# Optimization experiments

Measured on AMD Instinct MI355X. Metric: run time of the kernel, lower is better.

Reference implementation:

```python
import jax, jax.numpy as jnp
import numpy as np

B, Q, K = 4, 256, 1024          # batch, query_len, key_len
DQ, DK, DV, H = 512, 512, 512, 256  # query/key/value dims, num_hiddens


def setup_inputs() -> dict:
    key = jax.random.key(0)
    ks = jax.random.split(key, 7)
    return {
        "queries": jax.random.normal(ks[0], (B, Q, DQ), jnp.float32),
        "keys": jax.random.normal(ks[1], (B, K, DK), jnp.float32),
        "values": jax.random.normal(ks[2], (B, K, DV), jnp.float32),
        "valid_lens": jax.random.randint(ks[3], (B,), 1, K + 1),
        "Wq": jax.random.normal(ks[4], (H, DQ), jnp.float32) / np.sqrt(DQ).astype(np.float32),
        "Wk": jax.random.normal(ks[5], (H, DK), jnp.float32) / np.sqrt(DK).astype(np.float32),
        "wv": jax.random.normal(ks[6], (H,), jnp.float32) / np.sqrt(H).astype(np.float32),
    }


def reference(queries, keys, values, valid_lens, Wq, Wk, wv):
    # Linear projections (bias=False), torch Linear weight layout (out, in)
    q = jnp.einsum("bqd,hd->bqh", queries, Wq)          # (B, Q, H)
    k = jnp.einsum("bkd,hd->bkh", keys, Wk)             # (B, K, H)
    # Broadcast add -> tanh -> scalar score per (q, k) pair
    feats = jnp.tanh(q[:, :, None, :] + k[:, None, :, :])  # (B, Q, K, H)
    scores = jnp.einsum("bqkh,h->bqk", feats, wv)           # (B, Q, K)
    # masked_softmax with 1D valid_lens: mask applies along key axis per batch
    kv_len = scores.shape[-1]
    mask = jnp.arange(kv_len)[None, None, :] < valid_lens[:, None, None]  # (B,1,K)
    scores = jnp.where(mask, scores, jnp.float32(-1e6))
    attn = jax.nn.softmax(scores, axis=-1)               # (B, Q, K)
    # dropout is identity in eval mode
    return jnp.einsum("bqk,bkv->bqv", attn, values)      # (B, Q, DV)
```

## Files before the change

kernel.cpp:

```cpp
#include <hip/hip_runtime.h>
#include <stdint.h>


#define NB 4
#define NQ 256
#define NK 1024
#define ND 512
#define NH 256
#define QROWS 4
#define PJR 16
#define PJH 64

#define C2L2E 2.8853900817779268f
#define L2E   1.4426950408889634f

typedef float v2f __attribute__((ext_vector_type(2)));

__device__ void ff_vldec(const int* p, int* v) {
  bool ok = true;
  for (int i = 0; i < 4; ++i) { int x = p[i]; if (x < 1 || x > NK) ok = false; }
  if (ok) { for (int i = 0; i < 4; ++i) v[i] = p[i]; return; }
  ok = true;
  for (int i = 0; i < 4; ++i) {
    if (p[2 * i + 1] != 0) ok = false;
    int x = p[2 * i]; if (x < 1 || x > NK) ok = false;
  }
  if (ok) { for (int i = 0; i < 4; ++i) v[i] = p[2 * i]; return; }
  ok = true;
  for (int i = 0; i < 4; ++i) {
    union { int i; float f; } u; u.i = p[i];
    if (!(u.f >= 1.0f && u.f <= 1024.0f && u.f == floorf(u.f))) ok = false;
  }
  if (ok) {
    for (int i = 0; i < 4; ++i) { union { int i; float f; } u; u.i = p[i]; v[i] = (int)u.f; }
    return;
  }
  ok = true;
  for (int i = 0; i < 4; ++i) {
    union { long long l; double d; } u;
    u.l = ((long long)p[2 * i + 1] << 32) | (unsigned int)p[2 * i];
    if (!(u.d >= 1.0 && u.d <= 1024.0 && u.d == floor(u.d))) ok = false;
  }
  if (ok) {
    for (int i = 0; i < 4; ++i) {
      union { long long l; double d; } u;
      u.l = ((long long)p[2 * i + 1] << 32) | (unsigned int)p[2 * i];
      v[i] = (int)u.d;
    }
    return;
  }
  const uint16_t* hh = (const uint16_t*)p;
  const short*    s  = (const short*)p;
  ok = true;
  for (int i = 0; i < 4; ++i) { int x = s[i]; if (x < 1 || x > NK) ok = false; }
  if (ok) { for (int i = 0; i < 4; ++i) v[i] = s[i]; return; }
  ok = true;
  for (int i = 0; i < 4; ++i) {
    union { uint16_t u; _Float16 h; } u; u.u = hh[i];
    float f = (float)u.h;
    if (!(f >= 1.0f && f <= 1024.0f && f == floorf(f))) ok = false;
  }
  if (ok) {
    for (int i = 0; i < 4; ++i) {
      union { uint16_t u; _Float16 h; } u; u.u = hh[i];
      v[i] = (int)(float)u.h;
    }
    return;
  }
  ok = true;
  for (int i = 0; i < 4; ++i) {
    union { uint32_t u; float f; } u; u.u = ((uint32_t)hh[i]) << 16;
    if (!(u.f >= 1.0f && u.f <= 1028.0f)) ok = false;
  }
  if (ok) {
    for (int i = 0; i < 4; ++i) {
      union { uint32_t u; float f; } u; u.u = ((uint32_t)hh[i]) << 16;
      int x = (int)(u.f + 0.5f); if (x > NK) x = NK; v[i] = x;
    }
    return;
  }
  for (int i = 0; i < 4; ++i) v[i] = NK;
}

__global__ __launch_bounds__(256) void ff_wt(
    const float* __restrict__ Wq, const float* __restrict__ Wk,
    float* __restrict__ WTq, float* __restrict__ WTk)
{
  const int idx = blockIdx.x * 256 + threadIdx.x;
  const int d4 = idx & 127, h = idx >> 7;
  const float* src = blockIdx.y ? Wk : Wq;
  float*       dst = blockIdx.y ? WTk : WTq;
  float4 w = *(const float4*)(src + (size_t)h * ND + d4 * 4);
  w.x *= C2L2E; w.y *= C2L2E; w.z *= C2L2E; w.w *= C2L2E;
  *(float4*)(dst + ((size_t)d4 * NH + h) * 4) = w;
}

__global__ __launch_bounds__(256) void ff_proj(
    const float* __restrict__ q_in, const float* __restrict__ k_in,
    const float* __restrict__ WTq, const float* __restrict__ WTk,
    float* __restrict__ qp, float* __restrict__ kp)
{
  __shared__ float xs[PJR * ND];
  const int t  = threadIdx.x;
  const int rg = blockIdx.x >> 2;
  const int h0 = (blockIdx.x & 3) * PJH;
  const int gr0 = rg * PJR;
  const bool isq = gr0 < NB * NQ;
  const float* xin = isq ? (q_in + (size_t)gr0 * ND)
                         : (k_in + (size_t)(gr0 - NB * NQ) * ND);
  const float4* wt4 = (const float4*)(isq ? WTq : WTk);

  #pragma unroll
  for (int i = 0; i < 8; ++i)
    ((float4*)xs)[t + 256 * i] = ((const float4*)xin)[t + 256 * i];
  __syncthreads();

  const int L  = t & 63;
  const int rw = t >> 6;
  float a0 = 0.f, a1 = 0.f, a2 = 0.f, a3 = 0.f;
  const float4* xr = (const float4*)xs + (size_t)(4 * rw) * 128;

  #pragma unroll 4
  for (int d4 = 0; d4 < ND / 4; ++d4) {
    float4 w  = wt4[(size_t)d4 * NH + h0 + L];
    float4 x0 = xr[d4];
    float4 x1 = xr[128 + d4];
    float4 x2 = xr[256 + d4];
    float4 x3 = xr[384 + d4];
    a0 += w.x*x0.x + w.y*x0.y + w.z*x0.z + w.w*x0.w;
    a1 += w.x*x1.x + w.y*x1.y + w.z*x1.z + w.w*x1.w;
    a2 += w.x*x2.x + w.y*x2.y + w.z*x2.z + w.w*x2.w;
    a3 += w.x*x3.x + w.y*x3.y + w.z*x3.z + w.w*x3.w;
  }
  a0 = __builtin_amdgcn_exp2f(a0);
  a1 = __builtin_amdgcn_exp2f(a1);
  a2 = __builtin_amdgcn_exp2f(a2);
  a3 = __builtin_amdgcn_exp2f(a3);

  if (isq) {
    const int h = h0 + L;
    float* o = qp + (size_t)(gr0 + 4 * rw) * NH + h;
    o[0] = a0; o[NH] = a1; o[2 * NH] = a2; o[3 * NH] = a3;
  } else {
    __syncthreads();
    float* trs = xs;
    *(float4*)&trs[L * 16 + 4 * rw] = make_float4(a0, a1, a2, a3);
    __syncthreads();
    const int kl = t & 15, jl = t >> 4;
    const int g0 = gr0 - NB * NQ;
    const int bb = g0 >> 10, kg0 = g0 & (NK - 1);
    const int j0 = (blockIdx.x & 3) * 16;
    float4 o4 = make_float4(trs[(4*jl+0)*16 + kl], trs[(4*jl+1)*16 + kl],
                            trs[(4*jl+2)*16 + kl], trs[(4*jl+3)*16 + kl]);
    ((float4*)kp)[((size_t)bb * 64 + j0 + jl) * 1024 + kg0 + kl] = o4;
  }
}

__global__ __launch_bounds__(1024) void ff_attn4(
    const float* __restrict__ qp, const float* __restrict__ kp,
    const float* __restrict__ vals, const int* __restrict__ vlraw,
    const float* __restrict__ wvp, float* __restrict__ pvpart,
    float* __restrict__ Sg)
{
  __shared__ float  qs[QROWS * NH];
  __shared__ float4 wspp[NH / 2];
  __shared__ float  stp[2 * 256 * 4];
  __shared__ float  psum[16];
  __shared__ float  part[2 * 4 * 512];

  const int t  = threadIdx.x;
  const int ck = blockIdx.x;
  const int q0 = blockIdx.y * QROWS;
  const int b  = blockIdx.z;

  {
    qs[t] = qp[((size_t)b * NQ + q0) * NH + t];
    if (t < NH / 2) {
      float w0 = wvp[2 * t], w1 = wvp[2 * t + 1];
      wspp[t] = make_float4(-2.0f * w0, -2.0f * w1, -2.0f * (w0 + w1), 0.0f);
    }
  }
  __syncthreads();

  int vls[4];
  ff_vldec(vlraw, vls);
  const int vl = vls[b];

  const int kk = t & 255, rh = (t >> 8) & 1, hs = t >> 9;
  v2f acc = {0.f, 0.f};
  {
    const float4* kvp = (const float4*)kp + ((size_t)b * 64) * 1024
                      + (ck * 256 + kk);
    const float* q0p = qs + (2 * rh) * NH;
    const float* q1p = qs + (2 * rh + 1) * NH;
    #pragma unroll 4
    for (int jj = 0; jj < 32; ++jj) {
      const int j = hs * 32 + jj;
      float4 K4 = kvp[(size_t)j << 10];
      float4 A0 = *(const float4*)(q0p + 4 * j);
      float4 A1 = *(const float4*)(q1p + 4 * j);
      float4 wa = wspp[2 * j];
      float4 wb = wspp[2 * j + 1];
      v2f one; one.x = 1.0f; one.y = 1.0f;
      {
        v2f a;  a.x  = A0.x * K4.x; a.y  = A1.x * K4.x;
        v2f b2; b2.x = A0.y * K4.y; b2.y = A1.y * K4.y;
        v2f D = (one + a) * (one + b2);
        v2f N;   N.x = wa.z;  N.y = wa.z;
        v2f w0v; w0v.x = wa.x; w0v.y = wa.x;
        v2f w1v; w1v.x = wa.y; w1v.y = wa.y;
        N += w0v * b2;
        N += w1v * a;
        v2f rD;
        rD.x = __builtin_amdgcn_rcpf(D.x);
        rD.y = __builtin_amdgcn_rcpf(D.y);
        acc += N * rD;
      }
      {
        v2f a;  a.x  = A0.z * K4.z; a.y  = A1.z * K4.z;
        v2f b2; b2.x = A0.w * K4.w; b2.y = A1.w * K4.w;
        v2f D = (one + a) * (one + b2);
        v2f N;   N.x = wb.z;  N.y = wb.z;
        v2f w0v; w0v.x = wb.x; w0v.y = wb.x;
        v2f w1v; w1v.x = wb.y; w1v.y = wb.y;
        N += w0v * b2;
        N += w1v * a;
        v2f rD;
        rD.x = __builtin_amdgcn_rcpf(D.x);
        rD.y = __builtin_amdgcn_rcpf(D.y);
        acc += N * rD;
      }
    }
  }
  *(v2f*)&stp[(hs * 256 + kk) * 4 + 2 * rh] = acc;
  __syncthreads();

  {
    const int k = t & 255, row = t >> 8;
    float s = stp[k * 4 + row] + stp[(256 + k) * 4 + row];
    const bool okm = (ck * 256 + k) < vl;
    float E = okm ? __builtin_amdgcn_exp2f(s * L2E) : 0.f;
    stp[k * 4 + row] = E;
    float sx = E;
    for (int o = 32; o; o >>= 1) sx += __shfl_xor(sx, o);
    if ((t & 63) == 0) psum[t >> 6] = sx;
  }
  __syncthreads();
  if (t < 4) {
    float S = psum[t * 4] + psum[t * 4 + 1] + psum[t * 4 + 2] + psum[t * 4 + 3];
    Sg[((((size_t)b * 64 + blockIdx.y) * 4 + t)) * 4 + ck] = S;
  }

  {
    const int c = t & 511, kq = t >> 9;
    const float* vb = vals + (size_t)b * NK * ND
                    + (size_t)(ck * 256 + kq * 128) * ND + c;
    float o0 = 0.f, o1 = 0.f, o2 = 0.f, o3 = 0.f;
    #pragma unroll 8
    for (int k = 0; k < 128; ++k) {
      float v = vb[(size_t)k * ND];
      float4 a = *(const float4*)&stp[(kq * 128 + k) * 4];
      o0 += a.x * v; o1 += a.y * v; o2 += a.z * v; o3 += a.w * v;
    }
    part[(kq * 4 + 0) * 512 + c] = o0;
    part[(kq * 4 + 1) * 512 + c] = o1;
    part[(kq * 4 + 2) * 512 + c] = o2;
    part[(kq * 4 + 3) * 512 + c] = o3;
  }
  __syncthreads();
  {
    const int c = t & 511, rp = t >> 9;
    #pragma unroll
    for (int rr = 0; rr < 2; ++rr) {
      const int r = rp * 2 + rr;
      float s = part[(0 * 4 + r) * 512 + c] + part[(1 * 4 + r) * 512 + c];
      pvpart[((size_t)(ck * NB + b) * NQ + q0 + r) * ND + c] = s;
    }
  }
}

__global__ __launch_bounds__(256) void ff_comb(
    const float* __restrict__ pvpart, const float* __restrict__ Sg,
    float* __restrict__ out)
{
  const int bid = blockIdx.x;
  const int t = threadIdx.x;
  const float* sg = Sg + (size_t)bid * 4;
  const float S = (sg[0] + sg[1]) + (sg[2] + sg[3]);
  const float rs = 1.0f / S;
  const int b = bid >> 8, q = bid & 255;
  float2 acc = make_float2(0.f, 0.f);
  #pragma unroll
  for (int c = 0; c < 4; ++c) {
    const float* p = pvpart + ((size_t)(c * NB + b) * NQ + q) * ND;
    float2 v = *(const float2*)(p + t * 2);
    acc.x += v.x; acc.y += v.y;
  }
  *(float2*)(out + ((size_t)b * NQ + q) * ND + t * 2)
      = make_float2(acc.x * rs, acc.y * rs);
}

__global__ __launch_bounds__(1024) void ff_attn(
    const float* __restrict__ qp, const float* __restrict__ kp,
    const float* __restrict__ vals, const int* __restrict__ vlraw,
    const float* __restrict__ wvp, float* __restrict__ out)
{
  __shared__ float qs[QROWS * NH];
  __shared__ float ws[NH];
  __shared__ float st[NK * QROWS];
  __shared__ float pm[16], psm[16];
  __shared__ float part[4 * QROWS * ND];

  const int t  = threadIdx.x;
  const int q0 = blockIdx.x * QROWS;
  const int b  = blockIdx.y;

  {
    const float* qsrc = qp + ((size_t)b * NQ + q0) * NH;
    qs[t] = qsrc[t];
    if (t < NH) ws[t] = -2.0f * wvp[t];
  }
  __syncthreads();

  int vls[4];
  ff_vldec(vlraw, vls);
  const int vl = vls[b];

  float sc[4] = {0.f, 0.f, 0.f, 0.f};
  {
    const float4* kvp = (const float4*)kp + ((size_t)b * 64) * 1024 + t;
    for (int j = 0; j < 64; ++j) {
      float4 K4 = kvp[(size_t)j << 10];
      const float* wj = &ws[4 * j];
      #pragma unroll
      for (int r = 0; r < 4; ++r) {
        const float* qr = &qs[r * NH + 4 * j];
        sc[r] += wj[0] * __builtin_amdgcn_rcpf(1.0f + qr[0] * K4.x);
        sc[r] += wj[1] * __builtin_amdgcn_rcpf(1.0f + qr[1] * K4.y);
        sc[r] += wj[2] * __builtin_amdgcn_rcpf(1.0f + qr[2] * K4.z);
        sc[r] += wj[3] * __builtin_amdgcn_rcpf(1.0f + qr[3] * K4.w);
      }
    }
  }
  {
    const bool okm = (t < vl);
    *(float4*)&st[t * 4] = make_float4(okm ? sc[0] : -1e6f, okm ? sc[1] : -1e6f,
                                       okm ? sc[2] : -1e6f, okm ? sc[3] : -1e6f);
  }
  __syncthreads();

  {
    const int wid = t >> 6, lane = t & 63;
    const int row = wid >> 2, seg = wid & 3;
    const int kb = seg * 256 + lane;
    float v0 = st[(kb      ) * 4 + row];
    float v1 = st[(kb +  64) * 4 + row];
    float v2 = st[(kb + 128) * 4 + row];
    float v3 = st[(kb + 192) * 4 + row];
    float m = fmaxf(fmaxf(v0, v1), fmaxf(v2, v3));
    for (int o = 32; o; o >>= 1) m = fmaxf(m, __shfl_xor(m, o));
    if (lane == 0) pm[wid] = m;
    __syncthreads();
    m = fmaxf(fmaxf(pm[row*4+0], pm[row*4+1]), fmaxf(pm[row*4+2], pm[row*4+3]));
    float e0 = __builtin_amdgcn_exp2f((v0 - m) * L2E);
    float e1 = __builtin_amdgcn_exp2f((v1 - m) * L2E);
    float e2 = __builtin_amdgcn_exp2f((v2 - m) * L2E);
    float e3 = __builtin_amdgcn_exp2f((v3 - m) * L2E);
    float sm = e0 + e1 + e2 + e3;
    for (int o = 32; o; o >>= 1) sm += __shfl_xor(sm, o);
    if (lane == 0) psm[wid] = sm;
    __syncthreads();
    const float S = psm[row*4+0] + psm[row*4+1] + psm[row*4+2] + psm[row*4+3];
    const float rr = 1.0f / S;
    st[(kb      ) * 4 + row] = e0 * rr;
    st[(kb +  64) * 4 + row] = e1 * rr;
    st[(kb + 128) * 4 + row] = e2 * rr;
    st[(kb + 192) * 4 + row] = e3 * rr;
  }
  __syncthreads();

  {
    const int kq = t >> 8, c2 = (t & 255) * 2;
    const float* vb = vals + (size_t)b * NK * ND + c2;
    v2f o0 = {0.f,0.f}, o1 = {0.f,0.f}, o2 = {0.f,0.f}, o3 = {0.f,0.f};
    const int k0 = kq * 256;
    #pragma unroll 8
    for (int k = k0; k < k0 + 256; ++k) {
      v2f vv = *(const v2f*)(vb + (size_t)k * ND);
      float4 a = *(const float4*)&st[k * 4];
      v2f ax; ax.x = a.x; ax.y = a.x;
      v2f ay; ay.x = a.y; ay.y = a.y;
      v2f az; az.x = a.z; az.y = a.z;
      v2f aw; aw.x = a.w; aw.y = a.w;
      o0 += ax * vv; o1 += ay * vv; o2 += az * vv; o3 += aw * vv;
    }
    float* pp = &part[(size_t)kq * QROWS * ND + c2];
    *(v2f*)(pp         ) = o0;
    *(v2f*)(pp +     ND) = o1;
    *(v2f*)(pp + 2 * ND) = o2;
    *(v2f*)(pp + 3 * ND) = o3;
  }
  __syncthreads();
  {
    const int r = t >> 8, c2 = (t & 255) * 2;
    const float* pp = &part[(size_t)r * ND + c2];
    v2f s = {0.f, 0.f};
    #pragma unroll
    for (int kq = 0; kq < 4; ++kq) s += *(const v2f*)(pp + (size_t)kq * QROWS * ND);
    *(v2f*)(out + ((size_t)b * NQ + q0 + r) * ND + c2) = s;
  }
}

extern "C" void kernel_launch(void* const* d_in, const int* in_sizes, int n_in,
                              void* d_out, int out_size, void* d_ws, size_t ws_size,
                              hipStream_t stream) {
  const float* queries = (const float*)d_in[0];
  const float* keys    = (const float*)d_in[1];
  const float* values  = (const float*)d_in[2];
  const int*   vlens   = (const int*)d_in[3];
  const float* Wq      = (const float*)d_in[4];
  const float* Wk      = (const float*)d_in[5];
  const float* wv      = (const float*)d_in[6];
  float* out = (float*)d_out;

  float* qp  = (float*)d_ws;
  float* kp  = qp  + (size_t)NB * NQ * NH;
  float* wtq = kp  + (size_t)NB * NH * NK;
  float* wtk = wtq + (size_t)(ND / 4) * NH * 4;
  float* pvp = wtk + (size_t)(ND / 4) * NH * 4;
  float* Sg  = pvp + (size_t)4 * NB * NQ * ND;
  const size_t need = ((size_t)(Sg - (float*)d_ws) + 4 * NB * NQ) * sizeof(float);

  ff_wt  <<<dim3(128, 2), 256, 0, stream>>>(Wq, Wk, wtq, wtk);
  ff_proj<<<dim3((NB * (NQ + NK) / PJR) * (NH / PJH)), 256, 0, stream>>>(
      queries, keys, wtq, wtk, qp, kp);
  if (ws_size >= need) {
    ff_attn4<<<dim3(4, NQ / QROWS, NB), 1024, 0, stream>>>(
        qp, kp, values, vlens, wv, pvp, Sg);
    ff_comb<<<dim3(NB * NQ), 256, 0, stream>>>(pvp, Sg, out);
  } else {
    ff_attn<<<dim3(NQ / QROWS, NB), 1024, 0, stream>>>(
        qp, kp, values, vlens, wv, out);
  }
}
```

Before: 187.1 us.

## Split attention into score kernel and valid-length-bounded PV kernel

```diff
diff --git a/kernel.cpp b/kernel.cpp
--- a/kernel.cpp
+++ b/kernel.cpp
@@ -156,29 +156,24 @@
   }
 }
 
-__global__ __launch_bounds__(1024) void ff_attn4(
+__global__ __launch_bounds__(1024) void ff_attn_s(
     const float* __restrict__ qp, const float* __restrict__ kp,
-    const float* __restrict__ vals, const int* __restrict__ vlraw,
-    const float* __restrict__ wvp, float* __restrict__ pvpart,
-    float* __restrict__ Sg)
+    const int* __restrict__ vlraw, const float* __restrict__ wvp,
+    float* __restrict__ Eg, float* __restrict__ Sg)
 {
   __shared__ float  qs[QROWS * NH];
   __shared__ float4 wspp[NH / 2];
-  __shared__ float  stp[2 * 256 * 4];
-  __shared__ float  psum[16];
-  __shared__ float  part[2 * 4 * 512];
+  __shared__ float  pstp[2 * NK * 5];
+  __shared__ float  psum[16 * 4];
 
   const int t  = threadIdx.x;
-  const int ck = blockIdx.x;
-  const int q0 = blockIdx.y * QROWS;
-  const int b  = blockIdx.z;
-
-  {
-    qs[t] = qp[((size_t)b * NQ + q0) * NH + t];
-    if (t < NH / 2) {
-      float w0 = wvp[2 * t], w1 = wvp[2 * t + 1];
-      wspp[t] = make_float4(-2.0f * w0, -2.0f * w1, -2.0f * (w0 + w1), 0.0f);
-    }
+  const int q4 = blockIdx.x;
+  const int b  = blockIdx.y;
+
+  qs[t] = qp[((size_t)b * NQ + q4 * QROWS) * NH + t];
+  if (t < NH / 2) {
+    float w0 = wvp[2 * t], w1 = wvp[2 * t + 1];
+    wspp[t] = make_float4(-2.0f * w0, -2.0f * w1, -2.0f * (w0 + w1), 0.0f);
   }
   __syncthreads();
 
@@ -187,117 +182,143 @@
   const int vl = vls[b];
 
   const int kk = t & 255, rh = (t >> 8) & 1, hs = t >> 9;
-  v2f acc = {0.f, 0.f};
-  {
-    const float4* kvp = (const float4*)kp + ((size_t)b * 64) * 1024
-                      + (ck * 256 + kk);
+  const int k0 = kk * 4;
+
+  v2f acc0 = {0.f,0.f}, acc1 = {0.f,0.f}, acc2 = {0.f,0.f}, acc3 = {0.f,0.f};
+  {
+    const float4* kvp = (const float4*)kp + (size_t)b * 64 * 1024 + k0;
     const float* q0p = qs + (2 * rh) * NH;
     const float* q1p = qs + (2 * rh + 1) * NH;
-    #pragma unroll 4
+
+    #pragma unroll 2
     for (int jj = 0; jj < 32; ++jj) {
       const int j = hs * 32 + jj;
-      float4 K4 = kvp[(size_t)j << 10];
+      const float4* kj = kvp + ((size_t)j << 10);
+      float4 K0 = kj[0], K1 = kj[1], K2 = kj[2], K3 = kj[3];
       float4 A0 = *(const float4*)(q0p + 4 * j);
       float4 A1 = *(const float4*)(q1p + 4 * j);
       float4 wa = wspp[2 * j];
       float4 wb = wspp[2 * j + 1];
       v2f one; one.x = 1.0f; one.y = 1.0f;
-      {
-        v2f a;  a.x  = A0.x * K4.x; a.y  = A1.x * K4.x;
-        v2f b2; b2.x = A0.y * K4.y; b2.y = A1.y * K4.y;
-        v2f D = (one + a) * (one + b2);
-        v2f N;   N.x = wa.z;  N.y = wa.z;
-        v2f w0v; w0v.x = wa.x; w0v.y = wa.x;
-        v2f w1v; w1v.x = wa.y; w1v.y = wa.y;
-        N += w0v * b2;
-        N += w1v * a;
-        v2f rD;
-        rD.x = __builtin_amdgcn_rcpf(D.x);
-        rD.y = __builtin_amdgcn_rcpf(D.y);
-        acc += N * rD;
+
+#define FF_PAIRK(K4, ACC)                                                  \
+      {                                                                    \
+        v2f a, b2, D, N, w0v, w1v, rD;                                     \
+        a.x  = A0.x * K4.x; a.y  = A1.x * K4.x;                            \
+        b2.x = A0.y * K4.y; b2.y = A1.y * K4.y;                            \
+        D = (one + a) * (one + b2);                                        \
+        N.x = wa.z; N.y = wa.z;                                            \
+        w0v.x = wa.x; w0v.y = wa.x;                                        \
+        w1v.x = wa.y; w1v.y = wa.y;                                        \
+        N += w0v * b2; N += w1v * a;                                       \
+        rD.x = __builtin_amdgcn_rcpf(D.x);                                 \
+        rD.y = __builtin_amdgcn_rcpf(D.y);                                 \
+        ACC += N * rD;                                                     \
+        a.x  = A0.z * K4.z; a.y  = A1.z * K4.z;                            \
+        b2.x = A0.w * K4.w; b2.y = A1.w * K4.w;                            \
+        D = (one + a) * (one + b2);                                        \
+        N.x = wb.z; N.y = wb.z;                                            \
+        w0v.x = wb.x; w0v.y = wb.x;                                        \
+        w1v.x = wb.y; w1v.y = wb.y;                                        \
+        N += w0v * b2; N += w1v * a;                                       \
+        rD.x = __builtin_amdgcn_rcpf(D.x);                                 \
+        rD.y = __builtin_amdgcn_rcpf(D.y);                                 \
+        ACC += N * rD;                                                     \
       }
-      {
-        v2f a;  a.x  = A0.z * K4.z; a.y  = A1.z * K4.z;
-        v2f b2; b2.x = A0.w * K4.w; b2.y = A1.w * K4.w;
-        v2f D = (one + a) * (one + b2);
-        v2f N;   N.x = wb.z;  N.y = wb.z;
-        v2f w0v; w0v.x = wb.x; w0v.y = wb.x;
-        v2f w1v; w1v.x = wb.y; w1v.y = wb.y;
-        N += w0v * b2;
-        N += w1v * a;
-        v2f rD;
-        rD.x = __builtin_amdgcn_rcpf(D.x);
-        rD.y = __builtin_amdgcn_rcpf(D.y);
-        acc += N * rD;
-      }
-    }
-  }
-  *(v2f*)&stp[(hs * 256 + kk) * 4 + 2 * rh] = acc;
-  __syncthreads();
-
-  {
-    const int k = t & 255, row = t >> 8;
-    float s = stp[k * 4 + row] + stp[(256 + k) * 4 + row];
-    const bool okm = (ck * 256 + k) < vl;
-    float E = okm ? __builtin_amdgcn_exp2f(s * L2E) : 0.f;
-    stp[k * 4 + row] = E;
-    float sx = E;
-    for (int o = 32; o; o >>= 1) sx += __shfl_xor(sx, o);
-    if ((t & 63) == 0) psum[t >> 6] = sx;
+      FF_PAIRK(K0, acc0)
+      FF_PAIRK(K1, acc1)
+      FF_PAIRK(K2, acc2)
+      FF_PAIRK(K3, acc3)
+#undef FF_PAIRK
+    }
+  }
+
+  {
+    float* p = &pstp[(size_t)(hs * NK + k0) * 5 + 2 * rh];
+    p[0] = acc0.x; p[1] = acc0.y;
+    p[5] = acc1.x; p[6] = acc1.y;
+    p[10] = acc2.x; p[11] = acc2.y;
+    p[15] = acc3.x; p[16] = acc3.y;
+  }
+  __syncthreads();
+
+  {
+    const int k = t;
+    const float* p0 = &pstp[(size_t)k * 5];
+    const float* p1 = &pstp[(size_t)(NK + k) * 5];
+    const bool okm = k < vl;
+    float e0 = okm ? __builtin_amdgcn_exp2f((p0[0] + p1[0]) * L2E) : 0.f;
+    float e1 = okm ? __builtin_amdgcn_exp2f((p0[1] + p1[1]) * L2E) : 0.f;
+    float e2 = okm ? __builtin_amdgcn_exp2f((p0[2] + p1[2]) * L2E) : 0.f;
+    float e3 = okm ? __builtin_amdgcn_exp2f((p0[3] + p1[3]) * L2E) : 0.f;
+    ((float4*)Eg)[((size_t)b * 64 + q4) * NK + k] = make_float4(e0, e1, e2, e3);
+    float s0 = e0, s1 = e1, s2 = e2, s3 = e3;
+    for (int o = 32; o; o >>= 1) {
+      s0 += __shfl_xor(s0, o); s1 += __shfl_xor(s1, o);
+      s2 += __shfl_xor(s2, o); s3 += __shfl_xor(s3, o);
+    }
+    if ((t & 63) == 0)
+      *(float4*)&psum[(t >> 6) * 4] = make_float4(s0, s1, s2, s3);
   }
   __syncthreads();
   if (t < 4) {
-    float S = psum[t * 4] + psum[t * 4 + 1] + psum[t * 4 + 2] + psum[t * 4 + 3];
-    Sg[((((size_t)b * 64 + blockIdx.y) * 4 + t)) * 4 + ck] = S;
-  }
-
-  {
-    const int c = t & 511, kq = t >> 9;
-    const float* vb = vals + (size_t)b * NK * ND
-                    + (size_t)(ck * 256 + kq * 128) * ND + c;
-    float o0 = 0.f, o1 = 0.f, o2 = 0.f, o3 = 0.f;
-    #pragma unroll 8
-    for (int k = 0; k < 128; ++k) {
-      float v = vb[(size_t)k * ND];
-      float4 a = *(const float4*)&stp[(kq * 128 + k) * 4];
-      o0 += a.x * v; o1 += a.y * v; o2 += a.z * v; o3 += a.w * v;
-    }
-    part[(kq * 4 + 0) * 512 + c] = o0;
-    part[(kq * 4 + 1) * 512 + c] = o1;
-    part[(kq * 4 + 2) * 512 + c] = o2;
-    part[(kq * 4 + 3) * 512 + c] = o3;
-  }
-  __syncthreads();
-  {
-    const int c = t & 511, rp = t >> 9;
+    float S = 0.f;
     #pragma unroll
-    for (int rr = 0; rr < 2; ++rr) {
-      const int r = rp * 2 + rr;
-      float s = part[(0 * 4 + r) * 512 + c] + part[(1 * 4 + r) * 512 + c];
-      pvpart[((size_t)(ck * NB + b) * NQ + q0 + r) * ND + c] = s;
-    }
-  }
-}
-
-__global__ __launch_bounds__(256) void ff_comb(
-    const float* __restrict__ pvpart, const float* __restrict__ Sg,
+    for (int w = 0; w < 16; ++w) S += psum[w * 4 + t];
+    Sg[(((size_t)b * 64 + q4)) * 4 + t] = S;
+  }
+}
+
+__global__ __launch_bounds__(256) void ff_pv(
+    const float* __restrict__ vals, const float* __restrict__ Eg,
+    const float* __restrict__ Sg, const int* __restrict__ vlraw,
     float* __restrict__ out)
 {
-  const int bid = blockIdx.x;
-  const int t = threadIdx.x;
-  const float* sg = Sg + (size_t)bid * 4;
-  const float S = (sg[0] + sg[1]) + (sg[2] + sg[3]);
-  const float rs = 1.0f / S;
-  const int b = bid >> 8, q = bid & 255;
-  float2 acc = make_float2(0.f, 0.f);
-  #pragma unroll
-  for (int c = 0; c < 4; ++c) {
-    const float* p = pvpart + ((size_t)(c * NB + b) * NQ + q) * ND;
-    float2 v = *(const float2*)(p + t * 2);
-    acc.x += v.x; acc.y += v.y;
-  }
-  *(float2*)(out + ((size_t)b * NQ + q) * ND + t * 2)
-      = make_float2(acc.x * rs, acc.y * rs);
+  __shared__ float part[8 * 4 * 64];
+  const int t  = threadIdx.x;
+  const int ct = blockIdx.x;
+  const int q4 = blockIdx.y;
+  const int b  = blockIdx.z;
+
+  int vls[4];
+  ff_vldec(vlraw, vls);
+  const int vl = vls[b];
+
+  const int cl = t & 31, kq = t >> 5;
+  const int c  = ct * 64 + cl * 2;
+  const int k0 = kq * 128;
+  int klen = vl - k0; klen = klen < 0 ? 0 : (klen > 128 ? 128 : klen);
+
+  const float*  vb = vals + (size_t)b * NK * ND + (size_t)k0 * ND + c;
+  const float4* ep = (const float4*)Eg + ((size_t)b * 64 + q4) * NK + k0;
+
+  v2f a0 = {0.f,0.f}, a1 = {0.f,0.f}, a2 = {0.f,0.f}, a3 = {0.f,0.f};
+  #pragma unroll 4
+  for (int k = 0; k < klen; ++k) {
+    float4 E = ep[k];
+    v2f v = *(const v2f*)(vb + (size_t)k * ND);
+    v2f e;
+    e.x = E.x; e.y = E.x; a0 += e * v;
+    e.x = E.y; e.y = E.y; a1 += e * v;
+    e.x = E.z; e.y = E.z; a2 += e * v;
+    e.x = E.w; e.y = E.w; a3 += e * v;
+  }
+  {
+    float* pp = &part[(size_t)(kq * 4) * 64 + cl * 2];
+    *(v2f*)(pp      ) = a0;
+    *(v2f*)(pp + 64 ) = a1;
+    *(v2f*)(pp + 128) = a2;
+    *(v2f*)(pp + 192) = a3;
+  }
+  __syncthreads();
+  {
+    const int r = t >> 6, cc = t & 63;
+    float s = 0.f;
+    #pragma unroll
+    for (int q = 0; q < 8; ++q) s += part[(size_t)(q * 4 + r) * 64 + cc];
+    const float S = Sg[(((size_t)b * 64 + q4)) * 4 + r];
+    out[((size_t)b * NQ + q4 * QROWS + r) * ND + ct * 64 + cc] = s / S;
+  }
 }
 
 __global__ __launch_bounds__(1024) void ff_attn(
@@ -427,17 +448,18 @@
   float* kp  = qp  + (size_t)NB * NQ * NH;
   float* wtq = kp  + (size_t)NB * NH * NK;
   float* wtk = wtq + (size_t)(ND / 4) * NH * 4;
-  float* pvp = wtk + (size_t)(ND / 4) * NH * 4;
-  float* Sg  = pvp + (size_t)4 * NB * NQ * ND;
-  const size_t need = ((size_t)(Sg - (float*)d_ws) + 4 * NB * NQ) * sizeof(float);
+  float* Eg  = wtk + (size_t)(ND / 4) * NH * 4;
+  float* Sg  = Eg  + (size_t)NB * 64 * NK * 4;
+  const size_t need = ((size_t)(Sg - (float*)d_ws) + NB * 64 * 4) * sizeof(float);
 
   ff_wt  <<<dim3(128, 2), 256, 0, stream>>>(Wq, Wk, wtq, wtk);
   ff_proj<<<dim3((NB * (NQ + NK) / PJR) * (NH / PJH)), 256, 0, stream>>>(
       queries, keys, wtq, wtk, qp, kp);
   if (ws_size >= need) {
-    ff_attn4<<<dim3(4, NQ / QROWS, NB), 1024, 0, stream>>>(
-        qp, kp, values, vlens, wv, pvp, Sg);
-    ff_comb<<<dim3(NB * NQ), 256, 0, stream>>>(pvp, Sg, out);
+    ff_attn_s<<<dim3(NQ / QROWS, NB), 1024, 0, stream>>>(
+        qp, kp, vlens, wv, Eg, Sg);
+    ff_pv<<<dim3(8, NQ / QROWS, NB), 256, 0, stream>>>(
+        values, Eg, Sg, vlens, out);
   } else {
     ff_attn<<<dim3(NQ / QROWS, NB), 1024, 0, stream>>>(
         qp, kp, values, vlens, wv, out);
```

Measured after the change: 177.1 us. -5.4%, faster.
